# Performance work log

Measured on AMD Instinct MI355X. Metric: run time of the kernel, lower is better.

Reference implementation:

```python
import jax, jax.numpy as jnp
import numpy as np

T, B, D = 256, 256, 512
H, DK = 8, 64          # num_heads, d_kv; inner_dim = H*DK = 512
NUM_GROUPS = 16


def setup_inputs() -> dict:
    key = jax.random.key(0)
    ks = jax.random.split(key, 6)
    hidden_states = jax.random.normal(ks[0], (T, B, D), dtype=jnp.float32)
    # sorted group ids over the batch axis (what _infer_group_ids_from_mask recovers)
    group_ids = jnp.sort(jax.random.randint(ks[1], (B,), 0, NUM_GROUPS, dtype=jnp.int32))
    scale = 1.0 / np.sqrt(D)
    Wq = jax.random.normal(ks[2], (D, H * DK), dtype=jnp.float32) * scale
    Wk = jax.random.normal(ks[3], (D, H * DK), dtype=jnp.float32) * scale
    Wv = jax.random.normal(ks[4], (D, H * DK), dtype=jnp.float32) * scale
    Wo = jax.random.normal(ks[5], (H * DK, D), dtype=jnp.float32) * scale
    return {"hidden_states": hidden_states, "group_ids": group_ids,
            "Wq": Wq, "Wk": Wk, "Wv": Wv, "Wo": Wo}


def reference(hidden_states, group_ids, Wq, Wk, Wv, Wo):
    # Group-restricted self-attention along the batch axis, per time step & head.
    # Equivalent to the block-sparse MiniFlash kernel: entries attend only to
    # batch entries with the same group id.
    t, b, d = hidden_states.shape
    q = (hidden_states @ Wq).reshape(t, b, H, DK)
    k = (hidden_states @ Wk).reshape(t, b, H, DK)
    v = (hidden_states @ Wv).reshape(t, b, H, DK)
    sm_scale = 1.0 / np.sqrt(DK)
    # scores: [T, H, B, B] over the batch axis
    scores = jnp.einsum("tihd,tjhd->thij", q, k) * sm_scale
    allowed = group_ids[:, None] == group_ids[None, :]          # [B, B]
    neg = jnp.finfo(scores.dtype).min
    scores = jnp.where(allowed[None, None, :, :], scores, neg)
    attn = jax.nn.softmax(scores, axis=-1)
    out = jnp.einsum("thij,tjhd->tihd", attn, v).reshape(t, b, H * DK)
    return out @ Wo
```

## Files before the change

### kernel.cpp

```cpp
#include <hip/hip_runtime.h>
#include <hip/hip_bf16.h>

typedef __attribute__((ext_vector_type(8))) short short8;
typedef __attribute__((ext_vector_type(4))) short short4v;
typedef __attribute__((ext_vector_type(4))) float f32x4;

#define MFMA16(a, b, c) __builtin_amdgcn_mfma_f32_16x16x32_bf16(a, b, c, 0, 0, 0)

__device__ __forceinline__ unsigned short f2bf(float f) {
    union { __hip_bfloat16 h; unsigned short u; } v;
    v.h = __float2bfloat16(f);
    return v.u;
}

__device__ __forceinline__ short8 pack8(float4 a, float4 b) {
    short8 p;
    p[0] = (short)f2bf(a.x); p[1] = (short)f2bf(a.y);
    p[2] = (short)f2bf(a.z); p[3] = (short)f2bf(a.w);
    p[4] = (short)f2bf(b.x); p[5] = (short)f2bf(b.y);
    p[6] = (short)f2bf(b.z); p[7] = (short)f2bf(b.w);
    return p;
}

__device__ __forceinline__ int swz64(int row, int bytecol) {
    return row * 64 + ((bytecol ^ ((row & 7) << 4)) >> 1);
}
__device__ __forceinline__ int swz256(int row, int bytecol) {
    return row * 256 + ((bytecol ^ ((row & 7) << 4)) >> 1);
}

__device__ __forceinline__ void async16(void* lds_uniform, const void* gsrc) {
    __builtin_amdgcn_global_load_lds(
        (const __attribute__((address_space(1))) unsigned int*)gsrc,
        (__attribute__((address_space(3))) unsigned int*)lds_uniform,
        16, 0, 0);
}

__global__ __launch_bounds__(256) void wprep(
    const float* __restrict__ Wq, const float* __restrict__ Wk,
    const float* __restrict__ Wv, const float* __restrict__ Wo,
    unsigned short* __restrict__ wt, int swz)
{
    __shared__ float tile[64][65];
    const int bid = blockIdx.x;
    const int m = bid >> 6, tb = bid & 63;
    const int kr = (tb >> 3) << 6, nc = (tb & 7) << 6;
    const float* W = (m == 0) ? Wq : (m == 1) ? Wk : (m == 2) ? Wv : Wo;
    const int tid = threadIdx.x;
    for (int i = tid; i < 4096; i += 256)
        tile[i >> 6][i & 63] = W[(size_t)(kr + (i >> 6)) * 512 + nc + (i & 63)];
    __syncthreads();
    unsigned short* dst = wt + (size_t)m * 262144;
    for (int i = tid; i < 4096; i += 256) {
        const int n = nc + (i >> 6);
        const int e = i & 63;
        const int rsw = swz ? ((n & 7) * 8) : 0;
        dst[(size_t)n * 512 + kr + e] = f2bf(tile[e ^ rsw][i >> 6]);
    }
}

__global__ __launch_bounds__(256) void xprep(
    const float* __restrict__ hs, unsigned short* __restrict__ xb)
{
    const long long total = 4194304;
    for (long long g = (long long)blockIdx.x * 256 + threadIdx.x; g < total;
         g += (long long)gridDim.x * 256) {
        const int row = (int)(g >> 6);
        const int e0  = ((int)g & 63) * 8;
        const int src = e0 ^ ((row & 7) * 8);
        const float* s = hs + (size_t)row * 512 + src;
        const float4 f0 = *(const float4*)s;
        const float4 f1 = *(const float4*)(s + 4);
        *(short8*)(xb + (size_t)row * 512 + e0) = pack8(f0, f1);
    }
}

template<int F32OUT>
__global__ __launch_bounds__(256) void gemm_glds(
    const unsigned short* __restrict__ A,
    const unsigned short* __restrict__ B,
    unsigned short* __restrict__ obf,
    float* __restrict__ of32,
    int nbcnt)
{
    __shared__ unsigned short As[128 * 64];
    __shared__ unsigned short Bs[128 * 64];

    const int orig  = blockIdx.x;
    const int chunk = gridDim.x >> 3;
    const int wg = (orig & 7) * chunk + (orig >> 3);
    const int mb = wg / nbcnt;
    const int nb = wg - mb * nbcnt;

    const int tid  = threadIdx.x;
    const int lane = tid & 63;
    const int w    = tid >> 6;
    const int l15  = lane & 15;
    const int hi4  = lane >> 4;
    const int wr   = w >> 1, wc = w & 1;

    f32x4 acc[4][4];
    #pragma unroll
    for (int mt = 0; mt < 4; ++mt)
        #pragma unroll
        for (int nt = 0; nt < 4; ++nt)
            acc[mt][nt] = (f32x4){0.f, 0.f, 0.f, 0.f};

    const char* __restrict__ Ab = (const char*)(A + (size_t)mb * 128 * 512);
    const char* __restrict__ Bb = (const char*)(B + (size_t)nb * 128 * 512);
    const int sbase = w * 4096;

    for (int kb = 0; kb < 512; kb += 64) {
        #pragma unroll
        for (int i = 0; i < 4; ++i) {
            const int sb = sbase + i * 1024;
            const int s  = sb + lane * 16;
            const int row = s >> 7, colb = s & 127;
            const size_t goff = (size_t)row * 1024 + kb * 2 + colb;
            async16(&As[sb >> 1], Ab + goff);
            async16(&Bs[sb >> 1], Bb + goff);
        }
        __syncthreads();
        #pragma unroll
        for (int ks = 0; ks < 2; ++ks) {
            short8 af[4];
            #pragma unroll
            for (int mt = 0; mt < 4; ++mt)
                af[mt] = *(const short8*)&As[swz64(wr * 64 + mt * 16 + l15,
                                                   ks * 64 + hi4 * 16)];
            __builtin_amdgcn_s_setprio(1);
            #pragma unroll
            for (int nt = 0; nt < 4; ++nt) {
                const short8 bf = *(const short8*)&Bs[swz64(wc * 64 + nt * 16 + l15,
                                                            ks * 64 + hi4 * 16)];
                #pragma unroll
                for (int mt = 0; mt < 4; ++mt)
                    acc[mt][nt] = MFMA16(af[mt], bf, acc[mt][nt]);
            }
            __builtin_amdgcn_s_setprio(0);
        }
        __syncthreads();
    }

    #pragma unroll
    for (int mt = 0; mt < 4; ++mt) {
        #pragma unroll
        for (int nt = 0; nt < 4; ++nt) {
            const int colt = nb * 128 + wc * 64 + nt * 16 + l15;
            #pragma unroll
            for (int r = 0; r < 4; ++r) {
                const int row = mb * 128 + wr * 64 + mt * 16 + hi4 * 4 + r;
                if (F32OUT) {
                    of32[(size_t)row * 512 + colt] = acc[mt][nt][r];
                } else {
                    const int mat = colt >> 9, cc = colt & 511;
                    obf[(size_t)mat * 33554432 + (size_t)row * 512 + cc] =
                        f2bf(acc[mt][nt][r]);
                }
            }
        }
    }
}

__global__ __launch_bounds__(1024, 4) void qkv_gemm2(
    const float* __restrict__ hs,
    const unsigned short* __restrict__ wt,
    unsigned short* __restrict__ qkvb)
{
    __shared__ unsigned short As[128 * 64];
    __shared__ unsigned short Bts[512 * 64];

    const int orig = blockIdx.x;
    const int wg = (orig & 7) * 192 + (orig >> 3);
    const int mb = wg / 3;
    const int nb = wg - mb * 3;

    const int tid  = threadIdx.x;
    const int lane = tid & 63;
    const int w    = tid >> 6;
    const int l15  = lane & 15;
    const int hi4  = lane >> 4;
    const int wr   = w >> 3;
    const int wc   = w & 7;

    f32x4 acc[4][4];
    #pragma unroll
    for (int mt = 0; mt < 4; ++mt)
        #pragma unroll
        for (int nt = 0; nt < 4; ++nt)
            acc[mt][nt] = (f32x4){0.f, 0.f, 0.f, 0.f};

    const int ar = tid >> 3, aq = tid & 7;
    const int bc = tid >> 1, bh = tid & 1;
    const float* __restrict__ asrc = hs + ((size_t)mb * 128 + ar) * 512 + aq * 8;
    const unsigned short* __restrict__ bsrc =
        wt + ((size_t)nb * 512 + bc) * 512 + bh * 32;

    float4 a0, a1;
    short8 b8[4];
    a0 = *(const float4*)asrc;
    a1 = *(const float4*)(asrc + 4);
    #pragma unroll
    for (int q = 0; q < 4; ++q) b8[q] = *(const short8*)(bsrc + q * 8);

    for (int kb = 0; kb < 512; kb += 64) {
        *(short8*)&As[swz64(ar, aq * 16)] = pack8(a0, a1);
        #pragma unroll
        for (int q = 0; q < 4; ++q)
            *(short8*)&Bts[swz64(bc, bh * 64 + q * 16)] = b8[q];
        __syncthreads();
        if (kb < 448) {
            const int kn = kb + 64;
            a0 = *(const float4*)(asrc + kn);
            a1 = *(const float4*)(asrc + kn + 4);
            #pragma unroll
            for (int q = 0; q < 4; ++q)
                b8[q] = *(const short8*)(bsrc + kn + q * 8);
        }
        #pragma unroll
        for (int ks = 0; ks < 2; ++ks) {
            short8 af[4];
            #pragma unroll
            for (int mt = 0; mt < 4; ++mt)
                af[mt] = *(const short8*)&As[swz64(wr * 64 + mt * 16 + l15,
                                                   ks * 64 + hi4 * 16)];
            __builtin_amdgcn_s_setprio(1);
            #pragma unroll
            for (int nt = 0; nt < 4; ++nt) {
                const short8 bf = *(const short8*)&Bts[swz64(wc * 64 + nt * 16 + l15,
                                                             ks * 64 + hi4 * 16)];
                #pragma unroll
                for (int mt = 0; mt < 4; ++mt)
                    acc[mt][nt] = MFMA16(af[mt], bf, acc[mt][nt]);
            }
            __builtin_amdgcn_s_setprio(0);
        }
        __syncthreads();
    }

    unsigned short* __restrict__ dst = qkvb + (size_t)nb * 33554432ull;
    #pragma unroll
    for (int mt = 0; mt < 4; ++mt) {
        #pragma unroll
        for (int nt = 0; nt < 4; ++nt) {
            const int col = wc * 64 + nt * 16 + l15;
            #pragma unroll
            for (int r = 0; r < 4; ++r) {
                const int row = mb * 128 + wr * 64 + mt * 16 + hi4 * 4 + r;
                dst[(size_t)row * 512 + col] = f2bf(acc[mt][nt][r]);
            }
        }
    }
}

__global__ __launch_bounds__(1024, 4) void attn_split(
    unsigned short* __restrict__ qkvb,
    const int* __restrict__ gid,
    int doswz)
{
    __shared__ unsigned short Ksh[256 * 64];
    __shared__ unsigned short Vt[64 * 256];
    __shared__ unsigned short Ps[256 * 64];
    __shared__ int sgid[256];
    __shared__ int glo[16], ghi[16];

    const int th = blockIdx.x;
    const int t = th >> 3, h = th & 7;
    const int tid  = threadIdx.x;
    const int lane = tid & 63;
    const int w    = tid >> 6;
    const int l15  = lane & 15;
    const int hi4  = lane >> 4;
    const int wrow = w << 4;

    if (tid < 16) { glo[tid] = 256; ghi[tid] = -1; }
    __syncthreads();
    if (tid < 256) {
        const int g = gid[tid];
        sgid[tid] = g;
        atomicMin(&glo[g], tid);
        atomicMax(&ghi[g], tid);
    }

    const size_t rowbase = (size_t)t * 256 * 512 + h * 64;
    unsigned short* __restrict__ qb = qkvb + rowbase;
    const unsigned short* __restrict__ kbp = qkvb + 33554432ull + rowbase;
    const unsigned short* __restrict__ vbp = qkvb + 67108864ull + rowbase;

    {
        const int kr = tid >> 2, kq = tid & 3;
        const short8 k0 = *(const short8*)(kbp + (size_t)kr * 512 + kq * 16);
        const short8 k1 = *(const short8*)(kbp + (size_t)kr * 512 + kq * 16 + 8);
        *(short8*)&Ksh[swz64(kr, kq * 32)]      = k0;
        *(short8*)&Ksh[swz64(kr, kq * 32 + 16)] = k1;
        const short8 v0 = *(const short8*)(vbp + (size_t)kr * 512 + kq * 16);
        const short8 v1 = *(const short8*)(vbp + (size_t)kr * 512 + kq * 16 + 8);
        *(short8*)&Ps[kr * 64 + kq * 16]     = v0;
        *(short8*)&Ps[kr * 64 + kq * 16 + 8] = v1;
    }
    short8 qf[2];
    #pragma unroll
    for (int ks = 0; ks < 2; ++ks)
        qf[ks] = *(const short8*)(qb + (size_t)(wrow + l15) * 512 + ks * 32 + hi4 * 8);
    __syncthreads();

    {
        const int d = tid & 63, jc = tid >> 6;
        short8 a, b;
        #pragma unroll
        for (int jj = 0; jj < 8; ++jj) a[jj] = Ps[(jc * 16 + jj) * 64 + d];
        #pragma unroll
        for (int jj = 0; jj < 8; ++jj) b[jj] = Ps[(jc * 16 + 8 + jj) * 64 + d];
        *(short8*)&Vt[swz256(d, jc * 32)]      = a;
        *(short8*)&Vt[swz256(d, jc * 32 + 16)] = b;
    }
    __syncthreads();

    int rg[4];
    #pragma unroll
    for (int r = 0; r < 4; ++r) rg[r] = sgid[wrow + hi4 * 4 + r];
    const int klo = glo[sgid[wrow]];
    const int khi = ghi[sgid[wrow + 15]];

    f32x4 o[4];
    float mrun[4], lrun[4];
    #pragma unroll
    for (int n = 0; n < 4; ++n) o[n] = (f32x4){0.f, 0.f, 0.f, 0.f};
    #pragma unroll
    for (int r = 0; r < 4; ++r) { mrun[r] = -3.0e38f; lrun[r] = 0.f; }

    for (int kc = klo & ~63; kc <= khi; kc += 64) {
        f32x4 sfr[4];
        __builtin_amdgcn_s_setprio(1);
        #pragma unroll
        for (int n = 0; n < 4; ++n) {
            const int krow = kc + n * 16 + l15;
            const short8 kf0 = *(const short8*)&Ksh[swz64(krow, hi4 * 16)];
            const short8 kf1 = *(const short8*)&Ksh[swz64(krow, 64 + hi4 * 16)];
            f32x4 z = (f32x4){0.f, 0.f, 0.f, 0.f};
            z = MFMA16(qf[0], kf0, z);
            z = MFMA16(qf[1], kf1, z);
            sfr[n] = z;
        }
        __builtin_amdgcn_s_setprio(0);
        int cg[4];
        #pragma unroll
        for (int n = 0; n < 4; ++n) cg[n] = sgid[kc + n * 16 + l15];

        #pragma unroll
        for (int r = 0; r < 4; ++r) {
            const int gr = rg[r];
            float sv[4];
            float smax = -3.0e38f;
            #pragma unroll
            for (int n = 0; n < 4; ++n) {
                float x = sfr[n][r] * 0.125f;
                x = (cg[n] == gr) ? x : -3.0e38f;
                sv[n] = x;
                smax = fmaxf(smax, x);
            }
            smax = fmaxf(smax, __shfl_xor(smax, 1));
            smax = fmaxf(smax, __shfl_xor(smax, 2));
            smax = fmaxf(smax, __shfl_xor(smax, 4));
            smax = fmaxf(smax, __shfl_xor(smax, 8));
            const float newm = fmaxf(mrun[r], smax);
            const float corr = __expf(mrun[r] - newm);
            float ps = 0.f;
            unsigned short pb[4];
            #pragma unroll
            for (int n = 0; n < 4; ++n) {
                const float p = (sv[n] > -1.0e38f) ? __expf(sv[n] - newm) : 0.f;
                ps += p;
                pb[n] = f2bf(p);
            }
            ps += __shfl_xor(ps, 1); ps += __shfl_xor(ps, 2);
            ps += __shfl_xor(ps, 4); ps += __shfl_xor(ps, 8);
            lrun[r] = lrun[r] * corr + ps;
            mrun[r] = newm;
            #pragma unroll
            for (int n = 0; n < 4; ++n) o[n][r] *= corr;
            const int prow = wrow + hi4 * 4 + r;
            #pragma unroll
            for (int n = 0; n < 4; ++n)
                Ps[swz64(prow, (n * 16 + l15) * 2)] = pb[n];
        }

        const short8 pa0 = *(const short8*)&Ps[swz64(wrow + l15, hi4 * 16)];
        const short8 pa1 = *(const short8*)&Ps[swz64(wrow + l15, 64 + hi4 * 16)];
        __builtin_amdgcn_s_setprio(1);
        #pragma unroll
        for (int n = 0; n < 4; ++n) {
            const short8 vb0 = *(const short8*)&Vt[swz256(n * 16 + l15, (kc + hi4 * 8) * 2)];
            const short8 vb1 = *(const short8*)&Vt[swz256(n * 16 + l15, (kc + 32 + hi4 * 8) * 2)];
            o[n] = MFMA16(pa0, vb0, o[n]);
            o[n] = MFMA16(pa1, vb1, o[n]);
        }
        __builtin_amdgcn_s_setprio(0);
    }

    #pragma unroll
    for (int r = 0; r < 4; ++r) {
        const int row = wrow + hi4 * 4 + r;
        const float inv = 1.0f / lrun[r];
        const int rsw = doswz ? ((row & 7) * 8) : 0;
        #pragma unroll
        for (int n = 0; n < 4; ++n) {
            const int cc = n * 16 + l15;
            qb[(size_t)row * 512 + (cc ^ rsw)] = f2bf(o[n][r] * inv);
        }
    }
}

__global__ __launch_bounds__(1024, 4) void qkv_attn_mfma(
    const float* __restrict__ hs,
    const int*   __restrict__ gid,
    const float* __restrict__ Wq, const float* __restrict__ Wk,
    const float* __restrict__ Wv,
    float*       __restrict__ out)
{
    __shared__ unsigned short Xs[256 * 64];
    __shared__ unsigned short Wsh[192 * 64];
    __shared__ unsigned short Ksh[256 * 64];
    __shared__ unsigned short Vt[64 * 256];
    __shared__ unsigned short XP[256 * 64];
    __shared__ int sgid[256];
    __shared__ int glo[16], ghi[16];

    const int bid = blockIdx.x;
    const int h   = (bid & 63) >> 3;
    const int t   = ((bid >> 6) << 3) + (bid & 7);

    const int tid  = threadIdx.x;
    const int lane = tid & 63;
    const int w    = tid >> 6;
    const int l15  = lane & 15;
    const int hi4  = lane >> 4;
    const int mg   = w & 3;
    const int ng   = w >> 2;

    if (tid < 16) { glo[tid] = 256; ghi[tid] = -1; }
    __syncthreads();
    if (tid < 256) {
        const int g = gid[tid];
        sgid[tid] = g;
        atomicMin(&glo[g], tid);
        atomicMax(&ghi[g], tid);
    }

    const float* __restrict__ Xbase = hs + (size_t)t * (256 * 512);

    const int xr = tid >> 2, xq = tid & 3;
    const bool doW = tid < 768;
    const int wc = tid >> 2;
    const int wq = tid & 3;
    const int wmat = wc >> 6, wcol = wc & 63;
    const float* __restrict__ wfsrc =
        (wmat == 0) ? Wq : (wmat == 1) ? Wk : Wv;

    f32x4 acc[4][3];
    #pragma unroll
    for (int mt = 0; mt < 4; ++mt)
        #pragma unroll
        for (int nt = 0; nt < 3; ++nt)
            acc[mt][nt] = (f32x4){0.f, 0.f, 0.f, 0.f};

    float4 xf[4];
    short8 w8[2];
    {
        const float* s = Xbase + (size_t)xr * 512 + xq * 16;
        xf[0] = *(const float4*)(s + 0);  xf[1] = *(const float4*)(s + 4);
        xf[2] = *(const float4*)(s + 8);  xf[3] = *(const float4*)(s + 12);
        if (doW) {
            #pragma unroll
            for (int b = 0; b < 2; ++b)
                #pragma unroll
                for (int j = 0; j < 8; ++j)
                    w8[b][j] = (short)f2bf(
                        wfsrc[(size_t)(wq * 16 + b * 8 + j) * 512 + h * 64 + wcol]);
        }
    }

    for (int kb = 0; kb < 512; kb += 64) {
        *(short8*)&Xs[swz64(xr, xq * 32 + 0)]  = pack8(xf[0], xf[1]);
        *(short8*)&Xs[swz64(xr, xq * 32 + 16)] = pack8(xf[2], xf[3]);
        if (doW) {
            *(short8*)&Wsh[swz64(wc, wq * 32 + 0)]  = w8[0];
            *(short8*)&Wsh[swz64(wc, wq * 32 + 16)] = w8[1];
        }
        __syncthreads();
        if (kb < 448) {
            const int kn = kb + 64;
            const float* s = Xbase + (size_t)xr * 512 + kn + xq * 16;
            xf[0] = *(const float4*)(s + 0);  xf[1] = *(const float4*)(s + 4);
            xf[2] = *(const float4*)(s + 8);  xf[3] = *(const float4*)(s + 12);
            if (doW) {
                #pragma unroll
                for (int b = 0; b < 2; ++b)
                    #pragma unroll
                    for (int j = 0; j < 8; ++j)
                        w8[b][j] = (short)f2bf(
                            wfsrc[(size_t)(kn + wq * 16 + b * 8 + j) * 512 + h * 64 + wcol]);
            }
        }
        #pragma unroll
        for (int ks = 0; ks < 2; ++ks) {
            short8 af[4];
            #pragma unroll
            for (int mt = 0; mt < 4; ++mt)
                af[mt] = *(const short8*)&Xs[swz64(mg * 64 + mt * 16 + l15,
                                                   ks * 64 + hi4 * 16)];
            __builtin_amdgcn_s_setprio(1);
            #pragma unroll
            for (int nt = 0; nt < 3; ++nt) {
                const short8 bf = *(const short8*)&Wsh[swz64(ng * 48 + nt * 16 + l15,
                                                             ks * 64 + hi4 * 16)];
                #pragma unroll
                for (int mt = 0; mt < 4; ++mt)
                    acc[mt][nt] = MFMA16(af[mt], bf, acc[mt][nt]);
            }
            __builtin_amdgcn_s_setprio(0);
        }
        __syncthreads();
    }

    #pragma unroll
    for (int nt = 0; nt < 3; ++nt) {
        const int c0 = (ng * 3 + nt) * 16;
        const int m  = c0 >> 6;
        const int d0 = c0 & 63;
        #pragma unroll
        for (int mt = 0; mt < 4; ++mt) {
            const int rowb = mg * 64 + mt * 16 + hi4 * 4;
            if (m == 0) {
                #pragma unroll
                for (int r = 0; r < 4; ++r)
                    XP[swz64(rowb + r, (d0 + l15) * 2)] = f2bf(acc[mt][nt][r]);
            } else if (m == 1) {
                #pragma unroll
                for (int r = 0; r < 4; ++r)
                    Ksh[swz64(rowb + r, (d0 + l15) * 2)] = f2bf(acc[mt][nt][r]);
            } else {
                short4v vv;
                #pragma unroll
                for (int r = 0; r < 4; ++r) vv[r] = (short)f2bf(acc[mt][nt][r]);
                *(short4v*)&Vt[swz256(d0 + l15, rowb * 2)] = vv;
            }
        }
    }
    __syncthreads();

    const int wrow = w << 4;
    int rg[4];
    #pragma unroll
    for (int r = 0; r < 4; ++r) rg[r] = sgid[wrow + hi4 * 4 + r];
    const int klo = glo[sgid[wrow]];
    const int khi = ghi[sgid[wrow + 15]];

    short8 qf[2];
    #pragma unroll
    for (int ks = 0; ks < 2; ++ks)
        qf[ks] = *(const short8*)&XP[swz64(wrow + l15, ks * 64 + hi4 * 16)];

    f32x4 o[4];
    float mrun[4], lrun[4];
    #pragma unroll
    for (int n = 0; n < 4; ++n) o[n] = (f32x4){0.f, 0.f, 0.f, 0.f};
    #pragma unroll
    for (int r = 0; r < 4; ++r) { mrun[r] = -3.0e38f; lrun[r] = 0.f; }

    for (int kc = klo & ~63; kc <= khi; kc += 64) {
        f32x4 sfr[4];
        __builtin_amdgcn_s_setprio(1);
        #pragma unroll
        for (int n = 0; n < 4; ++n) {
            const int krow = kc + n * 16 + l15;
            const short8 kf0 = *(const short8*)&Ksh[swz64(krow, hi4 * 16)];
            const short8 kf1 = *(const short8*)&Ksh[swz64(krow, 64 + hi4 * 16)];
            f32x4 z = (f32x4){0.f, 0.f, 0.f, 0.f};
            z = MFMA16(qf[0], kf0, z);
            z = MFMA16(qf[1], kf1, z);
            sfr[n] = z;
        }
        __builtin_amdgcn_s_setprio(0);
        int cg[4];
        #pragma unroll
        for (int n = 0; n < 4; ++n) cg[n] = sgid[kc + n * 16 + l15];

        #pragma unroll
        for (int r = 0; r < 4; ++r) {
            const int gr = rg[r];
            float sv[4];
            float smax = -3.0e38f;
            #pragma unroll
            for (int n = 0; n < 4; ++n) {
                float x = sfr[n][r] * 0.125f;
                x = (cg[n] == gr) ? x : -3.0e38f;
                sv[n] = x;
                smax = fmaxf(smax, x);
            }
            smax = fmaxf(smax, __shfl_xor(smax, 1));
            smax = fmaxf(smax, __shfl_xor(smax, 2));
            smax = fmaxf(smax, __shfl_xor(smax, 4));
            smax = fmaxf(smax, __shfl_xor(smax, 8));
            const float newm = fmaxf(mrun[r], smax);
            const float corr = __expf(mrun[r] - newm);
            float ps = 0.f;
            unsigned short pb[4];
            #pragma unroll
            for (int n = 0; n < 4; ++n) {
                const float p = (sv[n] > -1.0e38f) ? __expf(sv[n] - newm) : 0.f;
                ps += p;
                pb[n] = f2bf(p);
            }
            ps += __shfl_xor(ps, 1); ps += __shfl_xor(ps, 2);
            ps += __shfl_xor(ps, 4); ps += __shfl_xor(ps, 8);
            lrun[r] = lrun[r] * corr + ps;
            mrun[r] = newm;
            #pragma unroll
            for (int n = 0; n < 4; ++n) o[n][r] *= corr;
            const int prow = wrow + hi4 * 4 + r;
            #pragma unroll
            for (int n = 0; n < 4; ++n)
                XP[swz64(prow, (n * 16 + l15) * 2)] = pb[n];
        }

        const short8 pa0 = *(const short8*)&XP[swz64(wrow + l15, hi4 * 16)];
        const short8 pa1 = *(const short8*)&XP[swz64(wrow + l15, 64 + hi4 * 16)];
        __builtin_amdgcn_s_setprio(1);
        #pragma unroll
        for (int n = 0; n < 4; ++n) {
            const short8 vb0 = *(const short8*)&Vt[swz256(n * 16 + l15, (kc + hi4 * 8) * 2)];
            const short8 vb1 = *(const short8*)&Vt[swz256(n * 16 + l15, (kc + 32 + hi4 * 8) * 2)];
            o[n] = MFMA16(pa0, vb0, o[n]);
            o[n] = MFMA16(pa1, vb1, o[n]);
        }
        __builtin_amdgcn_s_setprio(0);
    }

    float* __restrict__ op = out + (size_t)t * (256 * 512) + h * 64;
    #pragma unroll
    for (int r = 0; r < 4; ++r) {
        const int row = wrow + hi4 * 4 + r;
        const float inv = 1.0f / lrun[r];
        #pragma unroll
        for (int n = 0; n < 4; ++n)
            op[(size_t)row * 512 + n * 16 + l15] = o[n][r] * inv;
    }
}

__global__ __launch_bounds__(1024, 4) void oproj_mfma(
    const float* __restrict__ Wo,
    const unsigned short* __restrict__ wot,
    const unsigned short* __restrict__ abuf,
    float* __restrict__ out)
{
    __shared__ unsigned short As[128 * 40];
    __shared__ unsigned short Bts[512 * 40];

    const int tid  = threadIdx.x;
    const int lane = tid & 63;
    const int w    = tid >> 6;
    const int l15  = lane & 15;
    const int hi4  = lane >> 4;
    const int wr   = w >> 2;
    const int wc   = w & 3;
    const size_t r0 = (size_t)blockIdx.x * 128;

    f32x4 acc[2][8];
    #pragma unroll
    for (int m = 0; m < 2; ++m)
        #pragma unroll
        for (int n = 0; n < 8; ++n)
            acc[m][n] = (f32x4){0.f, 0.f, 0.f, 0.f};

    const bool isA = tid < 512;
    const int bn = tid & 511;
    const int ai = bn >> 2, aq = bn & 3;

    float4 af0, af1;
    short8 a8;
    short8 b8[4];

    if (isA) {
        if (abuf) {
            a8 = *(const short8*)(abuf + (r0 + ai) * 512 + aq * 8);
        } else {
            const float* s = out + (r0 + ai) * 512 + aq * 8;
            af0 = *(const float4*)s; af1 = *(const float4*)(s + 4);
        }
    } else {
        if (wot) {
            #pragma unroll
            for (int q = 0; q < 4; ++q)
                b8[q] = *(const short8*)(wot + (size_t)bn * 512 + q * 8);
        } else {
            #pragma unroll
            for (int q = 0; q < 4; ++q)
                #pragma unroll
                for (int j = 0; j < 8; ++j)
                    b8[q][j] = (short)f2bf(Wo[(size_t)(q * 8 + j) * 512 + bn]);
        }
    }

    for (int kb = 0; kb < 512; kb += 32) {
        if (isA) *(short8*)&As[ai * 40 + aq * 8] = abuf ? a8 : pack8(af0, af1);
        else {
            #pragma unroll
            for (int q = 0; q < 4; ++q)
                *(short8*)&Bts[bn * 40 + q * 8] = b8[q];
        }
        __syncthreads();
        if (kb < 480) {
            const int kn = kb + 32;
            if (isA) {
                if (abuf) {
                    a8 = *(const short8*)(abuf + (r0 + ai) * 512 + kn + aq * 8);
                } else {
                    const float* s = out + (r0 + ai) * 512 + kn + aq * 8;
                    af0 = *(const float4*)s; af1 = *(const float4*)(s + 4);
                }
            } else {
                if (wot) {
                    #pragma unroll
                    for (int q = 0; q < 4; ++q)
                        b8[q] = *(const short8*)(wot + (size_t)bn * 512 + kn + q * 8);
                } else {
                    #pragma unroll
                    for (int q = 0; q < 4; ++q)
                        #pragma unroll
                        for (int j = 0; j < 8; ++j)
                            b8[q][j] = (short)f2bf(Wo[(size_t)(kn + q * 8 + j) * 512 + bn]);
                }
            }
        }
        short8 afr[2];
        #pragma unroll
        for (int m = 0; m < 2; ++m)
            afr[m] = *(const short8*)&As[(wr * 32 + m * 16 + l15) * 40 + hi4 * 8];
        __builtin_amdgcn_s_setprio(1);
        #pragma unroll
        for (int n = 0; n < 8; ++n) {
            const short8 bfr = *(const short8*)&Bts[(wc * 128 + n * 16 + l15) * 40 + hi4 * 8];
            #pragma unroll
            for (int m = 0; m < 2; ++m)
                acc[m][n] = MFMA16(afr[m], bfr, acc[m][n]);
        }
        __builtin_amdgcn_s_setprio(0);
        __syncthreads();
    }

    #pragma unroll
    for (int m = 0; m < 2; ++m)
        #pragma unroll
        for (int n = 0; n < 8; ++n)
            #pragma unroll
            for (int r = 0; r < 4; ++r)
                out[(r0 + wr * 32 + m * 16 + hi4 * 4 + r) * 512 + wc * 128 + n * 16 + l15] =
                    acc[m][n][r];
}

extern "C" void kernel_launch(void* const* d_in, const int* in_sizes, int n_in,
                              void* d_out, int out_size, void* d_ws, size_t ws_size,
                              hipStream_t stream) {
    const float* hs  = (const float*)d_in[0];
    const int*   gid = (const int*)  d_in[1];
    const float* Wq  = (const float*)d_in[2];
    const float* Wk  = (const float*)d_in[3];
    const float* Wv  = (const float*)d_in[4];
    const float* Wo  = (const float*)d_in[5];
    float* outp = (float*)d_out;

    const size_t WT_S  = 1048576;
    const size_t XB_S  = 33554432;
    const size_t QKV_S = 100663296;
    unsigned short* wt = (unsigned short*)d_ws;
    unsigned short* wot = wt + (size_t)3 * 262144;

    if (ws_size >= (WT_S + XB_S + QKV_S) * 2) {
        unsigned short* xb   = wt + WT_S;
        unsigned short* qkvb = xb + XB_S;
        wprep<<<256, 256, 0, stream>>>(Wq, Wk, Wv, Wo, wt, 1);
        xprep<<<2048, 256, 0, stream>>>(hs, xb);
        gemm_glds<0><<<6144, 256, 0, stream>>>(xb, wt, qkvb, nullptr, 12);
        attn_split<<<2048, 1024, 0, stream>>>(qkvb, gid, 1);
        gemm_glds<1><<<2048, 256, 0, stream>>>(qkvb, wot, nullptr, outp, 4);
    } else if (ws_size >= (WT_S + QKV_S) * 2) {
        unsigned short* qkvb = wt + WT_S;
        wprep<<<256, 256, 0, stream>>>(Wq, Wk, Wv, Wo, wt, 0);
        qkv_gemm2<<<1536, 1024, 0, stream>>>(hs, wt, qkvb);
        attn_split<<<2048, 1024, 0, stream>>>(qkvb, gid, 0);
        oproj_mfma<<<512, 1024, 0, stream>>>(Wo, wot, qkvb, outp);
    } else {
        qkv_attn_mfma<<<2048, 1024, 0, stream>>>(hs, gid, Wq, Wk, Wv, outp);
        oproj_mfma<<<512, 1024, 0, stream>>>(Wo, nullptr, nullptr, outp);
    }
}
```

Before: 341.1 us.

## Restructure attention kernel to 512 threads with 32-row waves and narrower key chunks

Rewrites the per-(t,h) attention kernel to launch 512 threads, with each wave handling 32 query rows (two 16-row tiles) and iterating keys in 32-wide chunks instead of 64. The V transpose is now done straight from global memory into registers, which removes one LDS staging pass and one barrier. Group boundaries now come from a per-thread binary search over global gid, replacing the shared-memory atomics and their barrier. The aim is less LDS traffic and synchronisation, plus tighter key ranges that skip masked work. In exchange each wave carries more registers and issues more uncoalesced 4-byte global loads for V.

After: 345.0 us. Within noise of the previous version (+1.2%).

```diff
diff --git a/kernel.cpp b/kernel.cpp
--- a/kernel.cpp
+++ b/kernel.cpp
@@ -27,6 +27,9 @@
 }
 __device__ __forceinline__ int swz256(int row, int bytecol) {
     return row * 256 + ((bytecol ^ ((row & 7) << 4)) >> 1);
+}
+__device__ __forceinline__ int swz32(int row, int bytecol) {
+    return row * 32 + ((bytecol ^ ((row & 3) << 4)) >> 1);
 }
 
 __device__ __forceinline__ void async16(void* lds_uniform, const void* gsrc) {
@@ -116,7 +119,7 @@
             const int sb = sbase + i * 1024;
             const int s  = sb + lane * 16;
             const int row = s >> 7, colb = s & 127;
-            const size_t goff = (size_t)row * 1024 + kb * 2 + colb;
+            const size_t goff = (size_t)row * 1024 + (size_t)kb * 2 + colb;
             async16(&As[sb >> 1], Ab + goff);
             async16(&Bs[sb >> 1], Bb + goff);
         }
@@ -162,6 +165,189 @@
     }
 }
 
+__global__ __launch_bounds__(512, 4) void attn_split(
+    unsigned short* __restrict__ qkvb,
+    const int* __restrict__ gid,
+    int doswz)
+{
+    __shared__ unsigned short Ksh[256 * 64];
+    __shared__ unsigned short Vt[64 * 256];
+    __shared__ unsigned short Ps[256 * 32];
+
+    const int th = blockIdx.x;
+    const int t = th >> 3, h = th & 7;
+    const int tid  = threadIdx.x;
+    const int lane = tid & 63;
+    const int w    = tid >> 6;
+    const int l15  = lane & 15;
+    const int hi4  = lane >> 4;
+    const int wrow = w << 5;
+
+    const size_t rowbase = (size_t)t * 256 * 512 + h * 64;
+    unsigned short* __restrict__ qb = qkvb + rowbase;
+    const unsigned short* __restrict__ kbp = qkvb + 33554432ull + rowbase;
+    const unsigned short* __restrict__ vbp = qkvb + 67108864ull + rowbase;
+
+    {
+        const int kr = tid >> 1, kq = tid & 1;
+        #pragma unroll
+        for (int q = 0; q < 2; ++q) {
+            const short8 k0 = *(const short8*)(kbp + (size_t)kr * 512 + kq * 32 + q * 16);
+            const short8 k1 = *(const short8*)(kbp + (size_t)kr * 512 + kq * 32 + q * 16 + 8);
+            *(short8*)&Ksh[swz64(kr, kq * 64 + q * 32)]      = k0;
+            *(short8*)&Ksh[swz64(kr, kq * 64 + q * 32 + 16)] = k1;
+        }
+    }
+    {
+        const int d2 = (tid & 31) * 2;
+        const int jg = tid >> 5;
+        unsigned int vv[16];
+        #pragma unroll
+        for (int jj = 0; jj < 16; ++jj)
+            vv[jj] = *(const unsigned int*)(vbp + (size_t)(jg * 16 + jj) * 512 + d2);
+        short8 a0, a1, b0, b1;
+        #pragma unroll
+        for (int jj = 0; jj < 8; ++jj) {
+            a0[jj] = (short)(vv[jj] & 0xFFFFu);
+            b0[jj] = (short)(vv[jj] >> 16);
+            a1[jj] = (short)(vv[8 + jj] & 0xFFFFu);
+            b1[jj] = (short)(vv[8 + jj] >> 16);
+        }
+        *(short8*)&Vt[swz256(d2,     jg * 32)]      = a0;
+        *(short8*)&Vt[swz256(d2,     jg * 32 + 16)] = a1;
+        *(short8*)&Vt[swz256(d2 + 1, jg * 32)]      = b0;
+        *(short8*)&Vt[swz256(d2 + 1, jg * 32 + 16)] = b1;
+    }
+    short8 qf[2][2];
+    #pragma unroll
+    for (int a = 0; a < 2; ++a)
+        #pragma unroll
+        for (int ks = 0; ks < 2; ++ks)
+            qf[a][ks] = *(const short8*)(qb + (size_t)(wrow + a * 16 + l15) * 512 +
+                                          ks * 32 + hi4 * 8);
+
+    int rg[2][4];
+    #pragma unroll
+    for (int a = 0; a < 2; ++a)
+        #pragma unroll
+        for (int r = 0; r < 4; ++r)
+            rg[a][r] = gid[wrow + a * 16 + hi4 * 4 + r];
+    const int gfirst = gid[wrow], glast = gid[wrow + 31];
+    int lo = 0, hi2 = 256;
+    while (lo < hi2) { const int mid = (lo + hi2) >> 1;
+        if (gid[mid] < gfirst) lo = mid + 1; else hi2 = mid; }
+    const int klo = lo;
+    lo = 0; hi2 = 256;
+    while (lo < hi2) { const int mid = (lo + hi2) >> 1;
+        if (gid[mid] <= glast) lo = mid + 1; else hi2 = mid; }
+    const int khi = lo - 1;
+
+    __syncthreads();
+
+    f32x4 o[2][4];
+    float mrun[2][4], lrun[2][4];
+    #pragma unroll
+    for (int a = 0; a < 2; ++a)
+        #pragma unroll
+        for (int n = 0; n < 4; ++n)
+            o[a][n] = (f32x4){0.f, 0.f, 0.f, 0.f};
+    #pragma unroll
+    for (int a = 0; a < 2; ++a)
+        #pragma unroll
+        for (int r = 0; r < 4; ++r) { mrun[a][r] = -3.0e38f; lrun[a][r] = 0.f; }
+
+    for (int kc = klo & ~31; kc <= khi; kc += 32) {
+        f32x4 sfr[2][2];
+        __builtin_amdgcn_s_setprio(1);
+        #pragma unroll
+        for (int n = 0; n < 2; ++n) {
+            const int krow = kc + n * 16 + l15;
+            const short8 kf0 = *(const short8*)&Ksh[swz64(krow, hi4 * 16)];
+            const short8 kf1 = *(const short8*)&Ksh[swz64(krow, 64 + hi4 * 16)];
+            #pragma unroll
+            for (int a = 0; a < 2; ++a) {
+                f32x4 z = (f32x4){0.f, 0.f, 0.f, 0.f};
+                z = MFMA16(qf[a][0], kf0, z);
+                z = MFMA16(qf[a][1], kf1, z);
+                sfr[a][n] = z;
+            }
+        }
+        __builtin_amdgcn_s_setprio(0);
+        int cg[2];
+        #pragma unroll
+        for (int n = 0; n < 2; ++n) cg[n] = gid[kc + n * 16 + l15];
+
+        #pragma unroll
+        for (int a = 0; a < 2; ++a) {
+            #pragma unroll
+            for (int r = 0; r < 4; ++r) {
+                const int gr = rg[a][r];
+                float sv[2];
+                float smax = -3.0e38f;
+                #pragma unroll
+                for (int n = 0; n < 2; ++n) {
+                    float x = sfr[a][n][r] * 0.125f;
+                    x = (cg[n] == gr) ? x : -3.0e38f;
+                    sv[n] = x;
+                    smax = fmaxf(smax, x);
+                }
+                smax = fmaxf(smax, __shfl_xor(smax, 1));
+                smax = fmaxf(smax, __shfl_xor(smax, 2));
+                smax = fmaxf(smax, __shfl_xor(smax, 4));
+                smax = fmaxf(smax, __shfl_xor(smax, 8));
+                const float newm = fmaxf(mrun[a][r], smax);
+                const float corr = __expf(mrun[a][r] - newm);
+                float ps = 0.f;
+                unsigned short pb[2];
+                #pragma unroll
+                for (int n = 0; n < 2; ++n) {
+                    const float p = (sv[n] > -1.0e38f) ? __expf(sv[n] - newm) : 0.f;
+                    ps += p;
+                    pb[n] = f2bf(p);
+                }
+                ps += __shfl_xor(ps, 1); ps += __shfl_xor(ps, 2);
+                ps += __shfl_xor(ps, 4); ps += __shfl_xor(ps, 8);
+                lrun[a][r] = lrun[a][r] * corr + ps;
+                mrun[a][r] = newm;
+                #pragma unroll
+                for (int n = 0; n < 4; ++n) o[a][n][r] *= corr;
+                const int prow = wrow + a * 16 + hi4 * 4 + r;
+                #pragma unroll
+                for (int n = 0; n < 2; ++n)
+                    Ps[swz32(prow, (n * 16 + l15) * 2)] = pb[n];
+            }
+        }
+
+        __builtin_amdgcn_s_setprio(1);
+        #pragma unroll
+        for (int a = 0; a < 2; ++a) {
+            const short8 pa = *(const short8*)&Ps[swz32(wrow + a * 16 + l15, hi4 * 16)];
+            #pragma unroll
+            for (int n = 0; n < 4; ++n) {
+                const short8 vb = *(const short8*)&Vt[swz256(n * 16 + l15,
+                                                             (kc + hi4 * 8) * 2)];
+                o[a][n] = MFMA16(pa, vb, o[a][n]);
+            }
+        }
+        __builtin_amdgcn_s_setprio(0);
+    }
+
+    #pragma unroll
+    for (int a = 0; a < 2; ++a) {
+        #pragma unroll
+        for (int r = 0; r < 4; ++r) {
+            const int row = wrow + a * 16 + hi4 * 4 + r;
+            const float inv = 1.0f / lrun[a][r];
+            const int rsw = doswz ? ((row & 7) * 8) : 0;
+            #pragma unroll
+            for (int n = 0; n < 4; ++n) {
+                const int cc = n * 16 + l15;
+                qb[(size_t)row * 512 + (cc ^ rsw)] = f2bf(o[a][n][r] * inv);
+            }
+        }
+    }
+}
+
 __global__ __launch_bounds__(1024, 4) void qkv_gemm2(
     const float* __restrict__ hs,
     const unsigned short* __restrict__ wt,
@@ -249,164 +435,6 @@
                 const int row = mb * 128 + wr * 64 + mt * 16 + hi4 * 4 + r;
                 dst[(size_t)row * 512 + col] = f2bf(acc[mt][nt][r]);
             }
-        }
-    }
-}
-
-__global__ __launch_bounds__(1024, 4) void attn_split(
-    unsigned short* __restrict__ qkvb,
-    const int* __restrict__ gid,
-    int doswz)
-{
-    __shared__ unsigned short Ksh[256 * 64];
-    __shared__ unsigned short Vt[64 * 256];
-    __shared__ unsigned short Ps[256 * 64];
-    __shared__ int sgid[256];
-    __shared__ int glo[16], ghi[16];
-
-    const int th = blockIdx.x;
-    const int t = th >> 3, h = th & 7;
-    const int tid  = threadIdx.x;
-    const int lane = tid & 63;
-    const int w    = tid >> 6;
-    const int l15  = lane & 15;
-    const int hi4  = lane >> 4;
-    const int wrow = w << 4;
-
-    if (tid < 16) { glo[tid] = 256; ghi[tid] = -1; }
-    __syncthreads();
-    if (tid < 256) {
-        const int g = gid[tid];
-        sgid[tid] = g;
-        atomicMin(&glo[g], tid);
-        atomicMax(&ghi[g], tid);
-    }
-
-    const size_t rowbase = (size_t)t * 256 * 512 + h * 64;
-    unsigned short* __restrict__ qb = qkvb + rowbase;
-    const unsigned short* __restrict__ kbp = qkvb + 33554432ull + rowbase;
-    const unsigned short* __restrict__ vbp = qkvb + 67108864ull + rowbase;
-
-    {
-        const int kr = tid >> 2, kq = tid & 3;
-        const short8 k0 = *(const short8*)(kbp + (size_t)kr * 512 + kq * 16);
-        const short8 k1 = *(const short8*)(kbp + (size_t)kr * 512 + kq * 16 + 8);
-        *(short8*)&Ksh[swz64(kr, kq * 32)]      = k0;
-        *(short8*)&Ksh[swz64(kr, kq * 32 + 16)] = k1;
-        const short8 v0 = *(const short8*)(vbp + (size_t)kr * 512 + kq * 16);
-        const short8 v1 = *(const short8*)(vbp + (size_t)kr * 512 + kq * 16 + 8);
-        *(short8*)&Ps[kr * 64 + kq * 16]     = v0;
-        *(short8*)&Ps[kr * 64 + kq * 16 + 8] = v1;
-    }
-    short8 qf[2];
-    #pragma unroll
-    for (int ks = 0; ks < 2; ++ks)
-        qf[ks] = *(const short8*)(qb + (size_t)(wrow + l15) * 512 + ks * 32 + hi4 * 8);
-    __syncthreads();
-
-    {
-        const int d = tid & 63, jc = tid >> 6;
-        short8 a, b;
-        #pragma unroll
-        for (int jj = 0; jj < 8; ++jj) a[jj] = Ps[(jc * 16 + jj) * 64 + d];
-        #pragma unroll
-        for (int jj = 0; jj < 8; ++jj) b[jj] = Ps[(jc * 16 + 8 + jj) * 64 + d];
-        *(short8*)&Vt[swz256(d, jc * 32)]      = a;
-        *(short8*)&Vt[swz256(d, jc * 32 + 16)] = b;
-    }
-    __syncthreads();
-
-    int rg[4];
-    #pragma unroll
-    for (int r = 0; r < 4; ++r) rg[r] = sgid[wrow + hi4 * 4 + r];
-    const int klo = glo[sgid[wrow]];
-    const int khi = ghi[sgid[wrow + 15]];
-
-    f32x4 o[4];
-    float mrun[4], lrun[4];
-    #pragma unroll
-    for (int n = 0; n < 4; ++n) o[n] = (f32x4){0.f, 0.f, 0.f, 0.f};
-    #pragma unroll
-    for (int r = 0; r < 4; ++r) { mrun[r] = -3.0e38f; lrun[r] = 0.f; }
-
-    for (int kc = klo & ~63; kc <= khi; kc += 64) {
-        f32x4 sfr[4];
-        __builtin_amdgcn_s_setprio(1);
-        #pragma unroll
-        for (int n = 0; n < 4; ++n) {
-            const int krow = kc + n * 16 + l15;
-            const short8 kf0 = *(const short8*)&Ksh[swz64(krow, hi4 * 16)];
-            const short8 kf1 = *(const short8*)&Ksh[swz64(krow, 64 + hi4 * 16)];
-            f32x4 z = (f32x4){0.f, 0.f, 0.f, 0.f};
-            z = MFMA16(qf[0], kf0, z);
-            z = MFMA16(qf[1], kf1, z);
-            sfr[n] = z;
-        }
-        __builtin_amdgcn_s_setprio(0);
-        int cg[4];
-        #pragma unroll
-        for (int n = 0; n < 4; ++n) cg[n] = sgid[kc + n * 16 + l15];
-
-        #pragma unroll
-        for (int r = 0; r < 4; ++r) {
-            const int gr = rg[r];
-            float sv[4];
-            float smax = -3.0e38f;
-            #pragma unroll
-            for (int n = 0; n < 4; ++n) {
-                float x = sfr[n][r] * 0.125f;
-                x = (cg[n] == gr) ? x : -3.0e38f;
-                sv[n] = x;
-                smax = fmaxf(smax, x);
-            }
-            smax = fmaxf(smax, __shfl_xor(smax, 1));
-            smax = fmaxf(smax, __shfl_xor(smax, 2));
-            smax = fmaxf(smax, __shfl_xor(smax, 4));
-            smax = fmaxf(smax, __shfl_xor(smax, 8));
-            const float newm = fmaxf(mrun[r], smax);
-            const float corr = __expf(mrun[r] - newm);
-            float ps = 0.f;
-            unsigned short pb[4];
-            #pragma unroll
-            for (int n = 0; n < 4; ++n) {
-                const float p = (sv[n] > -1.0e38f) ? __expf(sv[n] - newm) : 0.f;
-                ps += p;
-                pb[n] = f2bf(p);
-            }
-            ps += __shfl_xor(ps, 1); ps += __shfl_xor(ps, 2);
-            ps += __shfl_xor(ps, 4); ps += __shfl_xor(ps, 8);
-            lrun[r] = lrun[r] * corr + ps;
-            mrun[r] = newm;
-            #pragma unroll
-            for (int n = 0; n < 4; ++n) o[n][r] *= corr;
-            const int prow = wrow + hi4 * 4 + r;
-            #pragma unroll
-            for (int n = 0; n < 4; ++n)
-                Ps[swz64(prow, (n * 16 + l15) * 2)] = pb[n];
-        }
-
-        const short8 pa0 = *(const short8*)&Ps[swz64(wrow + l15, hi4 * 16)];
-        const short8 pa1 = *(const short8*)&Ps[swz64(wrow + l15, 64 + hi4 * 16)];
-        __builtin_amdgcn_s_setprio(1);
-        #pragma unroll
-        for (int n = 0; n < 4; ++n) {
-            const short8 vb0 = *(const short8*)&Vt[swz256(n * 16 + l15, (kc + hi4 * 8) * 2)];
-            const short8 vb1 = *(const short8*)&Vt[swz256(n * 16 + l15, (kc + 32 + hi4 * 8) * 2)];
-            o[n] = MFMA16(pa0, vb0, o[n]);
-            o[n] = MFMA16(pa1, vb1, o[n]);
-        }
-        __builtin_amdgcn_s_setprio(0);
-    }
-
-    #pragma unroll
-    for (int r = 0; r < 4; ++r) {
-        const int row = wrow + hi4 * 4 + r;
-        const float inv = 1.0f / lrun[r];
-        const int rsw = doswz ? ((row & 7) * 8) : 0;
-        #pragma unroll
-        for (int n = 0; n < 4; ++n) {
-            const int cc = n * 16 + l15;
-            qb[(size_t)row * 512 + (cc ^ rsw)] = f2bf(o[n][r] * inv);
         }
     }
 }
@@ -782,13 +810,13 @@
         wprep<<<256, 256, 0, stream>>>(Wq, Wk, Wv, Wo, wt, 1);
         xprep<<<2048, 256, 0, stream>>>(hs, xb);
         gemm_glds<0><<<6144, 256, 0, stream>>>(xb, wt, qkvb, nullptr, 12);
-        attn_split<<<2048, 1024, 0, stream>>>(qkvb, gid, 1);
+        attn_split<<<2048, 512, 0, stream>>>(qkvb, gid, 1);
         gemm_glds<1><<<2048, 256, 0, stream>>>(qkvb, wot, nullptr, outp, 4);
     } else if (ws_size >= (WT_S + QKV_S) * 2) {
         unsigned short* qkvb = wt + WT_S;
         wprep<<<256, 256, 0, stream>>>(Wq, Wk, Wv, Wo, wt, 0);
         qkv_gemm2<<<1536, 1024, 0, stream>>>(hs, wt, qkvb);
-        attn_split<<<2048, 1024, 0, stream>>>(qkvb, gid, 0);
+        attn_split<<<2048, 512, 0, stream>>>(qkvb, gid, 0);
         oproj_mfma<<<512, 1024, 0, stream>>>(Wo, wot, qkvb, outp);
     } else {
         qkv_attn_mfma<<<2048, 1024, 0, stream>>>(hs, gid, Wq, Wk, Wv, outp);
```
